# Performance work log

Hardware: AMD Instinct MI355X
Metric: run time of the kernel (lower is better)

## Reference

```python
import jax, jax.numpy as jnp
import numpy as np

B, N_OP, N_MA, F, H, O = 32, 512, 64, 8, 128, 8


def _lin(k, fan_in, fan_out):
    kw, kb = jax.random.split(k)
    bound = 1.0 / np.sqrt(fan_in)
    w = jax.random.uniform(kw, (fan_in, fan_out), jnp.float32, -bound, bound)
    b = jax.random.uniform(kb, (fan_out,), jnp.float32, -bound, bound)
    return w, b


def setup_inputs() -> dict:
    key = jax.random.key(0)
    ks = jax.random.split(key, 12)
    inp = {
        "ope_ma_adj_batch": jax.random.randint(ks[0], (B, N_OP, N_MA), 0, 2, dtype=jnp.int32),
        "feats_op": jax.random.normal(ks[1], (B, N_OP, F), jnp.float32),
        "feats_ma": jax.random.normal(ks[2], (B, N_MA, F), jnp.float32),
    }
    # MLPsim 0 (machine aggregation): Linear(F,H), Linear(H,H), Linear(H,O)
    inp["l0_w1"], inp["l0_b1"] = _lin(ks[3], F, H)
    inp["l0_w2"], inp["l0_b2"] = _lin(ks[4], H, H)
    inp["l0_w3"], inp["l0_b3"] = _lin(ks[5], H, O)
    # MLPsim 1 (self-loop aggregation)
    inp["l1_w1"], inp["l1_b1"] = _lin(ks[6], F, H)
    inp["l1_w2"], inp["l1_b2"] = _lin(ks[7], H, H)
    inp["l1_w3"], inp["l1_b3"] = _lin(ks[8], H, O)
    # Final project: Linear(2*O,H), Linear(H,H), Linear(H,O)
    inp["p_w1"], inp["p_b1"] = _lin(ks[9], 2 * O, H)
    inp["p_w2"], inp["p_b2"] = _lin(ks[10], H, H)
    inp["p_w3"], inp["p_b3"] = _lin(ks[11], H, O)
    return inp


def _mlp3(x, w1, b1, w2, b2, w3, b3):
    # Linear -> ELU -> Linear -> ELU -> Linear (matches nn.Sequential in MLPsim.project)
    x = jax.nn.elu(x @ w1 + b1)
    x = jax.nn.elu(x @ w2 + b2)
    return x @ w3 + b3


def reference(ope_ma_adj_batch, feats_op, feats_ma,
              l0_w1, l0_b1, l0_w2, l0_b2, l0_w3, l0_b3,
              l1_w1, l1_b1, l1_w2, l1_b2, l1_w3, l1_b3,
              p_w1, p_b1, p_w2, p_b2, p_w3, p_b3):
    # MLPsim: adj.unsqueeze(-1)*feat.unsqueeze(-3) then sum(-2) == adj @ feat
    adj = ope_ma_adj_batch.astype(feats_ma.dtype)
    agg_ma = jnp.einsum('bnm,bmf->bnf', adj, feats_ma)       # (B, N_op, F)
    emb0 = _mlp3(agg_ma, l0_w1, l0_b1, l0_w2, l0_b2, l0_w3, l0_b3)
    # Second adjacency is the identity self-loop: I @ feats_op == feats_op
    emb1 = _mlp3(feats_op, l1_w1, l1_b1, l1_w2, l1_b2, l1_w3, l1_b3)
    cat = jnp.concatenate([emb0, emb1], axis=-1)              # (B, N_op, 2*O)
    # Final project: ELU -> Linear -> ELU -> Linear -> ELU -> Linear
    mu = _mlp3(jax.nn.elu(cat), p_w1, p_b1, p_w2, p_b2, p_w3, p_b3)
    return mu
```

## Files before the change

kernel.cpp:

```cpp
#include <hip/hip_runtime.h>

#define BB    32
#define N_OPC 512
#define N_MAC 64
#define FF    8
#define HH    128
#define OO    8
#define TM    32
#define ASTRB 136

typedef _Float16 f16x8 __attribute__((ext_vector_type(8)));
typedef _Float16 f16x4 __attribute__((ext_vector_type(4)));
typedef float    f32x4 __attribute__((ext_vector_type(4)));

#define WS_W2 0
#define WS_W3 49152
#define WS_W1 55296

__device__ __forceinline__ float elu_f(float x) {
    return x > 0.0f ? x : (__expf(x) - 1.0f);
}
__device__ __forceinline__ void store_f16(float v, ushort* dst, int off) {
    const _Float16 h = (_Float16)v;
    dst[off] = __builtin_bit_cast(ushort, h);
}

__global__ void prep_kernel(const float* __restrict__ w20, const float* __restrict__ w21,
                            const float* __restrict__ w22,
                            const float* __restrict__ w30, const float* __restrict__ w31,
                            const float* __restrict__ w32,
                            const float* __restrict__ w10, const float* __restrict__ w11,
                            const float* __restrict__ w12,
                            ushort* __restrict__ ws)
{
    const int gid = blockIdx.x * 256 + threadIdx.x;
    if (gid < 3 * 16384) {
        const int layer = gid >> 14, idx = gid & 16383;
        const float* w = layer == 0 ? w20 : layer == 1 ? w21 : w22;
        const int k = idx >> 7, j = idx & 127;
        const float x = w[idx];
        const int ks = k >> 5, kk = k & 31, jt = j >> 4, jj = j & 15;
        const int lane = ((kk >> 3) << 4) | jj, i = kk & 7;
        const int off = (((jt * 4 + ks) * 64 + lane) << 3) + i;
        const _Float16 h = (_Float16)x;
        ws[WS_W2 + layer * 16384 + off] = __builtin_bit_cast(ushort, h);
    } else if (gid < 3 * 16384 + 3 * 2048) {
        const int g2 = gid - 3 * 16384;
        const int layer = g2 >> 11, idx = g2 & 2047;
        const float* w = layer == 0 ? w30 : layer == 1 ? w31 : w32;
        const int i = idx & 7, lane = (idx >> 3) & 63, ks = idx >> 9;
        const int k = ks * 32 + (lane >> 4) * 8 + i, j = lane & 15;
        const float x = (j < OO) ? w[k * OO + j] : 0.0f;
        const _Float16 h = (_Float16)x;
        ws[WS_W3 + layer * 2048 + idx] = __builtin_bit_cast(ushort, h);
    } else {
        const int g1 = gid - (3 * 16384 + 3 * 2048);
        const int layer = g1 >> 12, idx = g1 & 4095;
        const float* w = layer == 0 ? w10 : layer == 1 ? w11 : w12;
        const int i = idx & 7, lane = (idx >> 3) & 63, jt = idx >> 9;
        const int k = (lane >> 4) * 8 + i, j = jt * 16 + (lane & 15);
        const int Kr = (layer == 2) ? 16 : 8;
        const float x = (k < Kr) ? w[k * HH + j] : 0.0f;
        const _Float16 h = (_Float16)x;
        ws[WS_W1 + layer * 4096 + idx] = __builtin_bit_cast(ushort, h);
    }
}

__device__ __forceinline__ void epi_store(f32x4 a, const float* __restrict__ bias, int jb,
                                          ushort* __restrict__ dst, int off)
{
    const float4 bb = *(const float4*)(bias + jb);
    f16x4 v;
    v[0] = (_Float16)elu_f(a[0] + bb.x);
    v[1] = (_Float16)elu_f(a[1] + bb.y);
    v[2] = (_Float16)elu_f(a[2] + bb.z);
    v[3] = (_Float16)elu_f(a[3] + bb.w);
    *(f16x4*)(dst + off) = v;
}

__global__ __launch_bounds__(512, 4) void mlps_kernel(
    const int*   __restrict__ adj,
    const float* __restrict__ fop,
    const float* __restrict__ fmab,
    const float* __restrict__ l0b1, const float* __restrict__ l0b2, const float* __restrict__ l0b3,
    const float* __restrict__ l1b1, const float* __restrict__ l1b2, const float* __restrict__ l1b3,
    const float* __restrict__ pb1,  const float* __restrict__ pb2,  const float* __restrict__ pb3,
    const ushort* __restrict__ wsf,
    float* __restrict__ out)
{
    __shared__ __align__(16) ushort hbuf[2][TM * ASTRB];
    __shared__ __align__(16) ushort gbuf[2][TM * ASTRB];
    __shared__ float fmS[N_MAC * FF];
    __shared__ __align__(16) ushort xinF[TM * FF];
    __shared__ __align__(16) ushort xopF[TM * FF];
    __shared__ __align__(16) ushort catF[TM * 16];

    const int tid  = threadIdx.x;
    const int wv   = tid >> 6;
    const int lane = tid & 63;
    const int lrow = lane & 15;
    const int lk   = lane >> 4;
    const int row0 = blockIdx.x * TM;
    const int b    = row0 / N_OPC;

    fmS[tid] = fmab[b * N_MAC * FF + tid];
    if (tid < TM * FF)
        store_f16(fop[row0 * FF + tid], xopF, tid);
    __syncthreads();

    if (tid < TM * FF) {
        const int r = tid >> 3, f = tid & 7;
        const int* arow = adj + (row0 + r) * N_MAC;
        float a = 0.0f;
        #pragma unroll
        for (int m4 = 0; m4 < N_MAC; m4 += 4) {
            const int4 av = *(const int4*)(arow + m4);
            a = fmaf((float)av.x, fmS[(m4 + 0) * FF + f], a);
            a = fmaf((float)av.y, fmS[(m4 + 1) * FF + f], a);
            a = fmaf((float)av.z, fmS[(m4 + 2) * FF + f], a);
            a = fmaf((float)av.w, fmS[(m4 + 3) * FF + f], a);
        }
        store_f16(a, xinF, tid);
    }
    __syncthreads();

    {
        const int br = wv >> 2, jt0 = (wv & 3) * 2;
        const ushort* xF = br ? xopF : xinF;
        const f16x8* WF = (const f16x8*)(wsf + WS_W1 + br * 4096);
        const float* b1 = br ? l1b1 : l0b1;
        f16x8 X[2] = {};
        if (lk == 0) {
            #pragma unroll
            for (int rt = 0; rt < 2; ++rt)
                X[rt] = *(const f16x8*)(xF + (rt * 16 + lrow) * 8);
        }
        f32x4 acc[2][2] = {};
        #pragma unroll
        for (int jtl = 0; jtl < 2; ++jtl) {
            const f16x8 wh = WF[(jt0 + jtl) * 64 + lane];
            #pragma unroll
            for (int rt = 0; rt < 2; ++rt)
                acc[jtl][rt] = __builtin_amdgcn_mfma_f32_16x16x32_f16(wh, X[rt], acc[jtl][rt], 0, 0, 0);
        }
        ushort* dF = hbuf[br];
        #pragma unroll
        for (int jtl = 0; jtl < 2; ++jtl) {
            const int jb = (jt0 + jtl) * 16 + lk * 4;
            #pragma unroll
            for (int rt = 0; rt < 2; ++rt)
                epi_store(acc[jtl][rt], b1, jb, dF, (rt * 16 + lrow) * ASTRB + jb);
        }
    }
    __syncthreads();

    {
        const int br = wv >> 2, jt0 = (wv & 3) * 2;
        const ushort* aF = hbuf[br];
        const f16x8* WF = (const f16x8*)(wsf + WS_W2 + br * 16384);
        f32x4 acc[2][2] = {};
        #pragma unroll
        for (int ks = 0; ks < 4; ++ks) {
            f16x8 x[2];
            #pragma unroll
            for (int rt = 0; rt < 2; ++rt)
                x[rt] = *(const f16x8*)(aF + (rt * 16 + lrow) * ASTRB + ks * 32 + lk * 8);
            #pragma unroll
            for (int jtl = 0; jtl < 2; ++jtl) {
                const f16x8 wh = WF[((jt0 + jtl) * 4 + ks) * 64 + lane];
                #pragma unroll
                for (int rt = 0; rt < 2; ++rt)
                    acc[jtl][rt] = __builtin_amdgcn_mfma_f32_16x16x32_f16(wh, x[rt], acc[jtl][rt], 0, 0, 0);
            }
        }
        const float* b2 = br ? l1b2 : l0b2;
        ushort* dF = gbuf[br];
        #pragma unroll
        for (int jtl = 0; jtl < 2; ++jtl) {
            const int jb = (jt0 + jtl) * 16 + lk * 4;
            #pragma unroll
            for (int rt = 0; rt < 2; ++rt)
                epi_store(acc[jtl][rt], b2, jb, dF, (rt * 16 + lrow) * ASTRB + jb);
        }
    }
    __syncthreads();

    if (wv < 4) {
        const int br = wv >> 1, rt = wv & 1;
        const ushort* aF = gbuf[br];
        const f16x8* WF = (const f16x8*)(wsf + WS_W3 + br * 2048);
        f32x4 acc = {};
        #pragma unroll
        for (int ks = 0; ks < 4; ++ks) {
            const f16x8 x = *(const f16x8*)(aF + (rt * 16 + lrow) * ASTRB + ks * 32 + lk * 8);
            const f16x8 wh = WF[ks * 64 + lane];
            acc = __builtin_amdgcn_mfma_f32_16x16x32_f16(wh, x, acc, 0, 0, 0);
        }
        if (lk < 2) {
            const float* b3 = br ? l1b3 : l0b3;
            epi_store(acc, b3, lk * 4, catF, (rt * 16 + lrow) * 16 + br * OO + lk * 4);
        }
    }
    __syncthreads();

    {
        const f16x8* WF = (const f16x8*)(wsf + WS_W1 + 2 * 4096);
        f16x8 X[2] = {};
        if (lk < 2) {
            #pragma unroll
            for (int rt = 0; rt < 2; ++rt)
                X[rt] = *(const f16x8*)(catF + (rt * 16 + lrow) * 16 + lk * 8);
        }
        f32x4 acc[2] = {};
        const f16x8 wh = WF[wv * 64 + lane];
        #pragma unroll
        for (int rt = 0; rt < 2; ++rt)
            acc[rt] = __builtin_amdgcn_mfma_f32_16x16x32_f16(wh, X[rt], acc[rt], 0, 0, 0);
        const int jb = wv * 16 + lk * 4;
        #pragma unroll
        for (int rt = 0; rt < 2; ++rt)
            epi_store(acc[rt], pb1, jb, hbuf[0], (rt * 16 + lrow) * ASTRB + jb);
    }
    __syncthreads();

    {
        const ushort* aF = hbuf[0];
        const f16x8* WF = (const f16x8*)(wsf + WS_W2 + 2 * 16384);
        f32x4 acc[2] = {};
        #pragma unroll
        for (int ks = 0; ks < 4; ++ks) {
            const f16x8 wh = WF[(wv * 4 + ks) * 64 + lane];
            #pragma unroll
            for (int rt = 0; rt < 2; ++rt) {
                const f16x8 x = *(const f16x8*)(aF + (rt * 16 + lrow) * ASTRB + ks * 32 + lk * 8);
                acc[rt] = __builtin_amdgcn_mfma_f32_16x16x32_f16(wh, x, acc[rt], 0, 0, 0);
            }
        }
        const int jb = wv * 16 + lk * 4;
        #pragma unroll
        for (int rt = 0; rt < 2; ++rt)
            epi_store(acc[rt], pb2, jb, gbuf[0], (rt * 16 + lrow) * ASTRB + jb);
    }
    __syncthreads();

    if (wv < 2) {
        const int rt = wv;
        const ushort* aF = gbuf[0];
        const f16x8* WF = (const f16x8*)(wsf + WS_W3 + 2 * 2048);
        f32x4 acc = {};
        #pragma unroll
        for (int ks = 0; ks < 4; ++ks) {
            const f16x8 x = *(const f16x8*)(aF + (rt * 16 + lrow) * ASTRB + ks * 32 + lk * 8);
            const f16x8 wh = WF[ks * 64 + lane];
            acc = __builtin_amdgcn_mfma_f32_16x16x32_f16(wh, x, acc, 0, 0, 0);
        }
        if (lk < 2) {
            const float4 bb = *(const float4*)(pb3 + lk * 4);
            float4 o;
            o.x = acc[0] + bb.x; o.y = acc[1] + bb.y;
            o.z = acc[2] + bb.z; o.w = acc[3] + bb.w;
            *(float4*)(out + (row0 + rt * 16 + lrow) * OO + lk * 4) = o;
        }
    }
}

extern "C" void kernel_launch(void* const* d_in, const int* in_sizes, int n_in,
                              void* d_out, int out_size, void* d_ws, size_t ws_size,
                              hipStream_t stream) {
    (void)in_sizes; (void)n_in; (void)out_size; (void)ws_size;
    const int*   adj  = (const int*)  d_in[0];
    const float* fop  = (const float*)d_in[1];
    const float* fmab = (const float*)d_in[2];
    const float* l0w1 = (const float*)d_in[3];
    const float* l0b1 = (const float*)d_in[4];
    const float* l0w2 = (const float*)d_in[5];
    const float* l0b2 = (const float*)d_in[6];
    const float* l0w3 = (const float*)d_in[7];
    const float* l0b3 = (const float*)d_in[8];
    const float* l1w1 = (const float*)d_in[9];
    const float* l1b1 = (const float*)d_in[10];
    const float* l1w2 = (const float*)d_in[11];
    const float* l1b2 = (const float*)d_in[12];
    const float* l1w3 = (const float*)d_in[13];
    const float* l1b3 = (const float*)d_in[14];
    const float* pw1  = (const float*)d_in[15];
    const float* pb1  = (const float*)d_in[16];
    const float* pw2  = (const float*)d_in[17];
    const float* pb2  = (const float*)d_in[18];
    const float* pw3  = (const float*)d_in[19];
    const float* pb3  = (const float*)d_in[20];
    float* out = (float*)d_out;
    ushort* wsf = (ushort*)d_ws;

    prep_kernel<<<dim3(264), dim3(256), 0, stream>>>(
        l0w2, l1w2, pw2, l0w3, l1w3, pw3, l0w1, l1w1, pw1, wsf);

    const int grid = (BB * N_OPC) / TM;
    mlps_kernel<<<dim3(grid), dim3(512), 0, stream>>>(
        adj, fop, fmab,
        l0b1, l0b2, l0b3,
        l1b1, l1b2, l1b3,
        pb1, pb2, pb3,
        wsf, out);
}
```

Before: 18.47 us.

## Fold machine features into first layer weights and prefetch weights into registers

The prep kernel now precomputes feats_ma @ W1 for each batch as an f16 fragment, so branch 0's first layer becomes a direct MFMA of the adjacency (converted to f16) against that product. This removes the scalar aggregation loop, the shared-memory staging of feats and two barriers. Weight fragments for later layers are loaded into registers one stage early so the global loads overlap the previous stage. In exchange the prep kernel does more work (about 1000 blocks), register pressure rises, and the reassociated sum is rounded to f16 before use.

Result: no change. 18.78 us (+1.7%).

```diff
diff --git a/kernel.cpp b/kernel.cpp
--- a/kernel.cpp
+++ b/kernel.cpp
@@ -13,16 +13,14 @@
 typedef _Float16 f16x4 __attribute__((ext_vector_type(4)));
 typedef float    f32x4 __attribute__((ext_vector_type(4)));
 
-#define WS_W2 0
-#define WS_W3 49152
-#define WS_W1 55296
+#define WS_W2  0
+#define WS_W3  49152
+#define WS_W1  55296
+#define WS_FMW 67584
+#define PREP_ITEMS (67584 + BB * 8192)
 
 __device__ __forceinline__ float elu_f(float x) {
     return x > 0.0f ? x : (__expf(x) - 1.0f);
-}
-__device__ __forceinline__ void store_f16(float v, ushort* dst, int off) {
-    const _Float16 h = (_Float16)v;
-    dst[off] = __builtin_bit_cast(ushort, h);
 }
 
 __global__ void prep_kernel(const float* __restrict__ w20, const float* __restrict__ w21,
@@ -31,6 +29,7 @@
                             const float* __restrict__ w32,
                             const float* __restrict__ w10, const float* __restrict__ w11,
                             const float* __restrict__ w12,
+                            const float* __restrict__ fmab,
                             ushort* __restrict__ ws)
 {
     const int gid = blockIdx.x * 256 + threadIdx.x;
@@ -53,7 +52,7 @@
         const float x = (j < OO) ? w[k * OO + j] : 0.0f;
         const _Float16 h = (_Float16)x;
         ws[WS_W3 + layer * 2048 + idx] = __builtin_bit_cast(ushort, h);
-    } else {
+    } else if (gid < 67584) {
         const int g1 = gid - (3 * 16384 + 3 * 2048);
         const int layer = g1 >> 12, idx = g1 & 4095;
         const float* w = layer == 0 ? w10 : layer == 1 ? w11 : w12;
@@ -63,6 +62,19 @@
         const float x = (k < Kr) ? w[k * HH + j] : 0.0f;
         const _Float16 h = (_Float16)x;
         ws[WS_W1 + layer * 4096 + idx] = __builtin_bit_cast(ushort, h);
+    } else {
+        const int g = gid - WS_FMW;
+        const int bb = g >> 13, idx = g & 8191;
+        const int i = idx & 7, lane = (idx >> 3) & 63, fk = idx >> 9;
+        const int ks = fk & 1, jt = fk >> 1;
+        const int k = ks * 32 + (lane >> 4) * 8 + i;
+        const int j = jt * 16 + (lane & 15);
+        const float* fmr = fmab + bb * (N_MAC * FF) + k * FF;
+        float x = 0.0f;
+        #pragma unroll
+        for (int f = 0; f < FF; ++f) x = fmaf(fmr[f], w10[f * HH + j], x);
+        const _Float16 h = (_Float16)x;
+        ws[WS_FMW + g] = __builtin_bit_cast(ushort, h);
     }
 }
 
@@ -81,7 +93,6 @@
 __global__ __launch_bounds__(512, 4) void mlps_kernel(
     const int*   __restrict__ adj,
     const float* __restrict__ fop,
-    const float* __restrict__ fmab,
     const float* __restrict__ l0b1, const float* __restrict__ l0b2, const float* __restrict__ l0b3,
     const float* __restrict__ l1b1, const float* __restrict__ l1b2, const float* __restrict__ l1b3,
     const float* __restrict__ pb1,  const float* __restrict__ pb2,  const float* __restrict__ pb3,
@@ -90,9 +101,6 @@
 {
     __shared__ __align__(16) ushort hbuf[2][TM * ASTRB];
     __shared__ __align__(16) ushort gbuf[2][TM * ASTRB];
-    __shared__ float fmS[N_MAC * FF];
-    __shared__ __align__(16) ushort xinF[TM * FF];
-    __shared__ __align__(16) ushort xopF[TM * FF];
     __shared__ __align__(16) ushort catF[TM * 16];
 
     const int tid  = threadIdx.x;
@@ -102,62 +110,93 @@
     const int lk   = lane >> 4;
     const int row0 = blockIdx.x * TM;
     const int b    = row0 / N_OPC;
-
-    fmS[tid] = fmab[b * N_MAC * FF + tid];
-    if (tid < TM * FF)
-        store_f16(fop[row0 * FF + tid], xopF, tid);
-    __syncthreads();
-
-    if (tid < TM * FF) {
-        const int r = tid >> 3, f = tid & 7;
-        const int* arow = adj + (row0 + r) * N_MAC;
-        float a = 0.0f;
-        #pragma unroll
-        for (int m4 = 0; m4 < N_MAC; m4 += 4) {
-            const int4 av = *(const int4*)(arow + m4);
-            a = fmaf((float)av.x, fmS[(m4 + 0) * FF + f], a);
-            a = fmaf((float)av.y, fmS[(m4 + 1) * FF + f], a);
-            a = fmaf((float)av.z, fmS[(m4 + 2) * FF + f], a);
-            a = fmaf((float)av.w, fmS[(m4 + 3) * FF + f], a);
-        }
-        store_f16(a, xinF, tid);
-    }
-    __syncthreads();
-
-    {
-        const int br = wv >> 2, jt0 = (wv & 3) * 2;
-        const ushort* xF = br ? xopF : xinF;
-        const f16x8* WF = (const f16x8*)(wsf + WS_W1 + br * 4096);
-        const float* b1 = br ? l1b1 : l0b1;
+    const int br   = wv >> 2, jt0 = (wv & 3) * 2;
+
+    f32x4 acc1[2][2] = {};
+    if (br == 0) {
+        const f16x8* FMWF = (const f16x8*)(wsf + WS_FMW + b * 8192);
+        f16x8 wa[2][2];
+        #pragma unroll
+        for (int jtl = 0; jtl < 2; ++jtl)
+            #pragma unroll
+            for (int ks = 0; ks < 2; ++ks)
+                wa[jtl][ks] = FMWF[((jt0 + jtl) * 2 + ks) * 64 + lane];
+        f16x8 xb[2][2];
+        #pragma unroll
+        for (int rt = 0; rt < 2; ++rt)
+            #pragma unroll
+            for (int ks = 0; ks < 2; ++ks) {
+                const int* ap = adj + (row0 + rt * 16 + lrow) * N_MAC + ks * 32 + lk * 8;
+                const int4 a0 = *(const int4*)ap;
+                const int4 a1 = *(const int4*)(ap + 4);
+                f16x8 v;
+                v[0] = (_Float16)a0.x; v[1] = (_Float16)a0.y;
+                v[2] = (_Float16)a0.z; v[3] = (_Float16)a0.w;
+                v[4] = (_Float16)a1.x; v[5] = (_Float16)a1.y;
+                v[6] = (_Float16)a1.z; v[7] = (_Float16)a1.w;
+                xb[rt][ks] = v;
+            }
+        #pragma unroll
+        for (int jtl = 0; jtl < 2; ++jtl)
+            #pragma unroll
+            for (int rt = 0; rt < 2; ++rt)
+                #pragma unroll
+                for (int ks = 0; ks < 2; ++ks)
+                    acc1[jtl][rt] = __builtin_amdgcn_mfma_f32_16x16x32_f16(wa[jtl][ks], xb[rt][ks], acc1[jtl][rt], 0, 0, 0);
+    } else {
+        const f16x8* WF = (const f16x8*)(wsf + WS_W1 + 4096);
+        const f16x8 w1a = WF[jt0 * 64 + lane];
+        const f16x8 w1b = WF[(jt0 + 1) * 64 + lane];
         f16x8 X[2] = {};
         if (lk == 0) {
             #pragma unroll
-            for (int rt = 0; rt < 2; ++rt)
-                X[rt] = *(const f16x8*)(xF + (rt * 16 + lrow) * 8);
-        }
-        f32x4 acc[2][2] = {};
-        #pragma unroll
-        for (int jtl = 0; jtl < 2; ++jtl) {
-            const f16x8 wh = WF[(jt0 + jtl) * 64 + lane];
-            #pragma unroll
-            for (int rt = 0; rt < 2; ++rt)
-                acc[jtl][rt] = __builtin_amdgcn_mfma_f32_16x16x32_f16(wh, X[rt], acc[jtl][rt], 0, 0, 0);
-        }
-        ushort* dF = hbuf[br];
+            for (int rt = 0; rt < 2; ++rt) {
+                const float* src = fop + (row0 + rt * 16 + lrow) * FF;
+                const float4 f0 = *(const float4*)src;
+                const float4 f1 = *(const float4*)(src + 4);
+                f16x8 v;
+                v[0] = (_Float16)f0.x; v[1] = (_Float16)f0.y;
+                v[2] = (_Float16)f0.z; v[3] = (_Float16)f0.w;
+                v[4] = (_Float16)f1.x; v[5] = (_Float16)f1.y;
+                v[6] = (_Float16)f1.z; v[7] = (_Float16)f1.w;
+                X[rt] = v;
+            }
+        }
+        #pragma unroll
+        for (int rt = 0; rt < 2; ++rt) {
+            acc1[0][rt] = __builtin_amdgcn_mfma_f32_16x16x32_f16(w1a, X[rt], acc1[0][rt], 0, 0, 0);
+            acc1[1][rt] = __builtin_amdgcn_mfma_f32_16x16x32_f16(w1b, X[rt], acc1[1][rt], 0, 0, 0);
+        }
+    }
+    f16x8 wf2[2][4];
+    {
+        const f16x8* W2F = (const f16x8*)(wsf + WS_W2 + br * 16384);
+        #pragma unroll
+        for (int jtl = 0; jtl < 2; ++jtl)
+            #pragma unroll
+            for (int ks = 0; ks < 4; ++ks)
+                wf2[jtl][ks] = W2F[((jt0 + jtl) * 4 + ks) * 64 + lane];
+    }
+    {
+        const float* b1 = br ? l1b1 : l0b1;
         #pragma unroll
         for (int jtl = 0; jtl < 2; ++jtl) {
             const int jb = (jt0 + jtl) * 16 + lk * 4;
             #pragma unroll
             for (int rt = 0; rt < 2; ++rt)
-                epi_store(acc[jtl][rt], b1, jb, dF, (rt * 16 + lrow) * ASTRB + jb);
-        }
-    }
-    __syncthreads();
-
-    {
-        const int br = wv >> 2, jt0 = (wv & 3) * 2;
+                epi_store(acc1[jtl][rt], b1, jb, hbuf[br], (rt * 16 + lrow) * ASTRB + jb);
+        }
+    }
+    __syncthreads();
+
+    f16x8 wf3[4];
+    if (wv < 4) {
+        const f16x8* WF3 = (const f16x8*)(wsf + WS_W3 + (wv >> 1) * 2048);
+        #pragma unroll
+        for (int ks = 0; ks < 4; ++ks) wf3[ks] = WF3[ks * 64 + lane];
+    }
+    {
         const ushort* aF = hbuf[br];
-        const f16x8* WF = (const f16x8*)(wsf + WS_W2 + br * 16384);
         f32x4 acc[2][2] = {};
         #pragma unroll
         for (int ks = 0; ks < 4; ++ks) {
@@ -166,45 +205,50 @@
             for (int rt = 0; rt < 2; ++rt)
                 x[rt] = *(const f16x8*)(aF + (rt * 16 + lrow) * ASTRB + ks * 32 + lk * 8);
             #pragma unroll
-            for (int jtl = 0; jtl < 2; ++jtl) {
-                const f16x8 wh = WF[((jt0 + jtl) * 4 + ks) * 64 + lane];
+            for (int jtl = 0; jtl < 2; ++jtl)
                 #pragma unroll
                 for (int rt = 0; rt < 2; ++rt)
-                    acc[jtl][rt] = __builtin_amdgcn_mfma_f32_16x16x32_f16(wh, x[rt], acc[jtl][rt], 0, 0, 0);
-            }
+                    acc[jtl][rt] = __builtin_amdgcn_mfma_f32_16x16x32_f16(wf2[jtl][ks], x[rt], acc[jtl][rt], 0, 0, 0);
         }
         const float* b2 = br ? l1b2 : l0b2;
-        ushort* dF = gbuf[br];
         #pragma unroll
         for (int jtl = 0; jtl < 2; ++jtl) {
             const int jb = (jt0 + jtl) * 16 + lk * 4;
             #pragma unroll
             for (int rt = 0; rt < 2; ++rt)
-                epi_store(acc[jtl][rt], b2, jb, dF, (rt * 16 + lrow) * ASTRB + jb);
-        }
-    }
-    __syncthreads();
-
+                epi_store(acc[jtl][rt], b2, jb, gbuf[br], (rt * 16 + lrow) * ASTRB + jb);
+        }
+    }
+    __syncthreads();
+
+    f16x8 wf4;
+    {
+        const f16x8* WF = (const f16x8*)(wsf + WS_W1 + 2 * 4096);
+        wf4 = WF[wv * 64 + lane];
+    }
     if (wv < 4) {
-        const int br = wv >> 1, rt = wv & 1;
-        const ushort* aF = gbuf[br];
-        const f16x8* WF = (const f16x8*)(wsf + WS_W3 + br * 2048);
+        const int br3 = wv >> 1, rt = wv & 1;
+        const ushort* aF = gbuf[br3];
         f32x4 acc = {};
         #pragma unroll
         for (int ks = 0; ks < 4; ++ks) {
             const f16x8 x = *(const f16x8*)(aF + (rt * 16 + lrow) * ASTRB + ks * 32 + lk * 8);
-            const f16x8 wh = WF[ks * 64 + lane];
-            acc = __builtin_amdgcn_mfma_f32_16x16x32_f16(wh, x, acc, 0, 0, 0);
+            acc = __builtin_amdgcn_mfma_f32_16x16x32_f16(wf3[ks], x, acc, 0, 0, 0);
         }
         if (lk < 2) {
-            const float* b3 = br ? l1b3 : l0b3;
-            epi_store(acc, b3, lk * 4, catF, (rt * 16 + lrow) * 16 + br * OO + lk * 4);
-        }
-    }
-    __syncthreads();
-
-    {
-        const f16x8* WF = (const f16x8*)(wsf + WS_W1 + 2 * 4096);
+            const float* b3 = br3 ? l1b3 : l0b3;
+            epi_store(acc, b3, lk * 4, catF, (rt * 16 + lrow) * 16 + br3 * OO + lk * 4);
+        }
+    }
+    __syncthreads();
+
+    f16x8 wf5[4];
+    {
+        const f16x8* WF = (const f16x8*)(wsf + WS_W2 + 2 * 16384);
+        #pragma unroll
+        for (int ks = 0; ks < 4; ++ks) wf5[ks] = WF[(wv * 4 + ks) * 64 + lane];
+    }
+    {
         f16x8 X[2] = {};
         if (lk < 2) {
             #pragma unroll
@@ -212,10 +256,9 @@
                 X[rt] = *(const f16x8*)(catF + (rt * 16 + lrow) * 16 + lk * 8);
         }
         f32x4 acc[2] = {};
-        const f16x8 wh = WF[wv * 64 + lane];
         #pragma unroll
         for (int rt = 0; rt < 2; ++rt)
-            acc[rt] = __builtin_amdgcn_mfma_f32_16x16x32_f16(wh, X[rt], acc[rt], 0, 0, 0);
+            acc[rt] = __builtin_amdgcn_mfma_f32_16x16x32_f16(wf4, X[rt], acc[rt], 0, 0, 0);
         const int jb = wv * 16 + lk * 4;
         #pragma unroll
         for (int rt = 0; rt < 2; ++rt)
@@ -223,17 +266,21 @@
     }
     __syncthreads();
 
+    f16x8 wf6[4];
+    if (wv < 2) {
+        const f16x8* WF = (const f16x8*)(wsf + WS_W3 + 2 * 2048);
+        #pragma unroll
+        for (int ks = 0; ks < 4; ++ks) wf6[ks] = WF[ks * 64 + lane];
+    }
     {
         const ushort* aF = hbuf[0];
-        const f16x8* WF = (const f16x8*)(wsf + WS_W2 + 2 * 16384);
         f32x4 acc[2] = {};
         #pragma unroll
         for (int ks = 0; ks < 4; ++ks) {
-            const f16x8 wh = WF[(wv * 4 + ks) * 64 + lane];
             #pragma unroll
             for (int rt = 0; rt < 2; ++rt) {
                 const f16x8 x = *(const f16x8*)(aF + (rt * 16 + lrow) * ASTRB + ks * 32 + lk * 8);
-                acc[rt] = __builtin_amdgcn_mfma_f32_16x16x32_f16(wh, x, acc[rt], 0, 0, 0);
+                acc[rt] = __builtin_amdgcn_mfma_f32_16x16x32_f16(wf5[ks], x, acc[rt], 0, 0, 0);
             }
         }
         const int jb = wv * 16 + lk * 4;
@@ -246,13 +293,11 @@
     if (wv < 2) {
         const int rt = wv;
         const ushort* aF = gbuf[0];
-        const f16x8* WF = (const f16x8*)(wsf + WS_W3 + 2 * 2048);
         f32x4 acc = {};
         #pragma unroll
         for (int ks = 0; ks < 4; ++ks) {
             const f16x8 x = *(const f16x8*)(aF + (rt * 16 + lrow) * ASTRB + ks * 32 + lk * 8);
-            const f16x8 wh = WF[ks * 64 + lane];
-            acc = __builtin_amdgcn_mfma_f32_16x16x32_f16(wh, x, acc, 0, 0, 0);
+            acc = __builtin_amdgcn_mfma_f32_16x16x32_f16(wf6[ks], x, acc, 0, 0, 0);
         }
         if (lk < 2) {
             const float4 bb = *(const float4*)(pb3 + lk * 4);
@@ -292,12 +337,13 @@
     float* out = (float*)d_out;
     ushort* wsf = (ushort*)d_ws;
 
-    prep_kernel<<<dim3(264), dim3(256), 0, stream>>>(
-        l0w2, l1w2, pw2, l0w3, l1w3, pw3, l0w1, l1w1, pw1, wsf);
+    const int prep_blocks = PREP_ITEMS / 256;
+    prep_kernel<<<dim3(prep_blocks), dim3(256), 0, stream>>>(
+        l0w2, l1w2, pw2, l0w3, l1w3, pw3, l0w1, l1w1, pw1, fmab, wsf);
 
     const int grid = (BB * N_OPC) / TM;
     mlps_kernel<<<dim3(grid), dim3(512), 0, stream>>>(
-        adj, fop, fmab,
+        adj, fop,
         l0b1, l0b2, l0b3,
         l1b1, l1b2, l1b3,
         pb1, pb2, pb3,
```

## Drop weight-prep kernel; gather fp32 weights into fp16 MFMA fragments in-kernel

Applied to the files above, without the earlier changes.

Removes the separate prep kernel that repacked weights into fp16 MFMA-fragment layout in the workspace. Each wave now gathers its weight fragments directly from the fp32 weight tensors with strided scalar loads and converts them to fp16. Most fragments are prefetched before the layer that uses them, and the layer-2 fragments are loaded before the adjacency aggregation. This saves one kernel launch and its serialization, but adds many uncoalesced strided global loads per block (512 blocks each re-gathering weights), plus more register pressure from holding the fragments.

New measurement: 17.77 us (median of 2 runs). 1.04x faster.

```diff
diff --git a/kernel.cpp b/kernel.cpp
--- a/kernel.cpp
+++ b/kernel.cpp
@@ -13,10 +13,6 @@
 typedef _Float16 f16x4 __attribute__((ext_vector_type(4)));
 typedef float    f32x4 __attribute__((ext_vector_type(4)));
 
-#define WS_W2 0
-#define WS_W3 49152
-#define WS_W1 55296
-
 __device__ __forceinline__ float elu_f(float x) {
     return x > 0.0f ? x : (__expf(x) - 1.0f);
 }
@@ -24,46 +20,12 @@
     const _Float16 h = (_Float16)v;
     dst[off] = __builtin_bit_cast(ushort, h);
 }
-
-__global__ void prep_kernel(const float* __restrict__ w20, const float* __restrict__ w21,
-                            const float* __restrict__ w22,
-                            const float* __restrict__ w30, const float* __restrict__ w31,
-                            const float* __restrict__ w32,
-                            const float* __restrict__ w10, const float* __restrict__ w11,
-                            const float* __restrict__ w12,
-                            ushort* __restrict__ ws)
-{
-    const int gid = blockIdx.x * 256 + threadIdx.x;
-    if (gid < 3 * 16384) {
-        const int layer = gid >> 14, idx = gid & 16383;
-        const float* w = layer == 0 ? w20 : layer == 1 ? w21 : w22;
-        const int k = idx >> 7, j = idx & 127;
-        const float x = w[idx];
-        const int ks = k >> 5, kk = k & 31, jt = j >> 4, jj = j & 15;
-        const int lane = ((kk >> 3) << 4) | jj, i = kk & 7;
-        const int off = (((jt * 4 + ks) * 64 + lane) << 3) + i;
-        const _Float16 h = (_Float16)x;
-        ws[WS_W2 + layer * 16384 + off] = __builtin_bit_cast(ushort, h);
-    } else if (gid < 3 * 16384 + 3 * 2048) {
-        const int g2 = gid - 3 * 16384;
-        const int layer = g2 >> 11, idx = g2 & 2047;
-        const float* w = layer == 0 ? w30 : layer == 1 ? w31 : w32;
-        const int i = idx & 7, lane = (idx >> 3) & 63, ks = idx >> 9;
-        const int k = ks * 32 + (lane >> 4) * 8 + i, j = lane & 15;
-        const float x = (j < OO) ? w[k * OO + j] : 0.0f;
-        const _Float16 h = (_Float16)x;
-        ws[WS_W3 + layer * 2048 + idx] = __builtin_bit_cast(ushort, h);
-    } else {
-        const int g1 = gid - (3 * 16384 + 3 * 2048);
-        const int layer = g1 >> 12, idx = g1 & 4095;
-        const float* w = layer == 0 ? w10 : layer == 1 ? w11 : w12;
-        const int i = idx & 7, lane = (idx >> 3) & 63, jt = idx >> 9;
-        const int k = (lane >> 4) * 8 + i, j = jt * 16 + (lane & 15);
-        const int Kr = (layer == 2) ? 16 : 8;
-        const float x = (k < Kr) ? w[k * HH + j] : 0.0f;
-        const _Float16 h = (_Float16)x;
-        ws[WS_W1 + layer * 4096 + idx] = __builtin_bit_cast(ushort, h);
-    }
+__device__ __forceinline__ f16x8 gather8(const float* __restrict__ w, int kbase, int j, int ld) {
+    f16x8 v;
+    #pragma unroll
+    for (int i = 0; i < 8; ++i)
+        v[i] = (_Float16)w[(kbase + i) * ld + j];
+    return v;
 }
 
 __device__ __forceinline__ void epi_store(f32x4 a, const float* __restrict__ bias, int jb,
@@ -82,10 +44,15 @@
     const int*   __restrict__ adj,
     const float* __restrict__ fop,
     const float* __restrict__ fmab,
-    const float* __restrict__ l0b1, const float* __restrict__ l0b2, const float* __restrict__ l0b3,
-    const float* __restrict__ l1b1, const float* __restrict__ l1b2, const float* __restrict__ l1b3,
-    const float* __restrict__ pb1,  const float* __restrict__ pb2,  const float* __restrict__ pb3,
-    const ushort* __restrict__ wsf,
+    const float* __restrict__ l0w1, const float* __restrict__ l0b1,
+    const float* __restrict__ l0w2, const float* __restrict__ l0b2,
+    const float* __restrict__ l0w3, const float* __restrict__ l0b3,
+    const float* __restrict__ l1w1, const float* __restrict__ l1b1,
+    const float* __restrict__ l1w2, const float* __restrict__ l1b2,
+    const float* __restrict__ l1w3, const float* __restrict__ l1b3,
+    const float* __restrict__ pw1,  const float* __restrict__ pb1,
+    const float* __restrict__ pw2,  const float* __restrict__ pb2,
+    const float* __restrict__ pw3,  const float* __restrict__ pb3,
     float* __restrict__ out)
 {
     __shared__ __align__(16) ushort hbuf[2][TM * ASTRB];
@@ -102,6 +69,21 @@
     const int lk   = lane >> 4;
     const int row0 = blockIdx.x * TM;
     const int b    = row0 / N_OPC;
+    const int br   = wv >> 2, jt0 = (wv & 3) * 2;
+
+    const float* w1p = br ? l1w1 : l0w1;
+    f16x8 w1f[2] = {};
+    if (lk == 0) {
+        w1f[0] = gather8(w1p, 0, jt0 * 16 + lrow, HH);
+        w1f[1] = gather8(w1p, 0, (jt0 + 1) * 16 + lrow, HH);
+    }
+    const float* w2p = br ? l1w2 : l0w2;
+    f16x8 wf2[2][4];
+    #pragma unroll
+    for (int jtl = 0; jtl < 2; ++jtl)
+        #pragma unroll
+        for (int ks = 0; ks < 4; ++ks)
+            wf2[jtl][ks] = gather8(w2p, ks * 32 + lk * 8, (jt0 + jtl) * 16 + lrow, HH);
 
     fmS[tid] = fmab[b * N_MAC * FF + tid];
     if (tid < TM * FF)
@@ -125,9 +107,7 @@
     __syncthreads();
 
     {
-        const int br = wv >> 2, jt0 = (wv & 3) * 2;
         const ushort* xF = br ? xopF : xinF;
-        const f16x8* WF = (const f16x8*)(wsf + WS_W1 + br * 4096);
         const float* b1 = br ? l1b1 : l0b1;
         f16x8 X[2] = {};
         if (lk == 0) {
@@ -137,27 +117,29 @@
         }
         f32x4 acc[2][2] = {};
         #pragma unroll
-        for (int jtl = 0; jtl < 2; ++jtl) {
-            const f16x8 wh = WF[(jt0 + jtl) * 64 + lane];
-            #pragma unroll
-            for (int rt = 0; rt < 2; ++rt)
-                acc[jtl][rt] = __builtin_amdgcn_mfma_f32_16x16x32_f16(wh, X[rt], acc[jtl][rt], 0, 0, 0);
-        }
-        ushort* dF = hbuf[br];
+        for (int jtl = 0; jtl < 2; ++jtl)
+            #pragma unroll
+            for (int rt = 0; rt < 2; ++rt)
+                acc[jtl][rt] = __builtin_amdgcn_mfma_f32_16x16x32_f16(w1f[jtl], X[rt], acc[jtl][rt], 0, 0, 0);
         #pragma unroll
         for (int jtl = 0; jtl < 2; ++jtl) {
             const int jb = (jt0 + jtl) * 16 + lk * 4;
             #pragma unroll
             for (int rt = 0; rt < 2; ++rt)
-                epi_store(acc[jtl][rt], b1, jb, dF, (rt * 16 + lrow) * ASTRB + jb);
-        }
-    }
-    __syncthreads();
-
-    {
-        const int br = wv >> 2, jt0 = (wv & 3) * 2;
+                epi_store(acc[jtl][rt], b1, jb, hbuf[br], (rt * 16 + lrow) * ASTRB + jb);
+        }
+    }
+    __syncthreads();
+
+    f16x8 wf3[4] = {};
+    if (wv < 4 && lrow < OO) {
+        const float* w3p = (wv >> 1) ? l1w3 : l0w3;
+        #pragma unroll
+        for (int ks = 0; ks < 4; ++ks)
+            wf3[ks] = gather8(w3p, ks * 32 + lk * 8, lrow, OO);
+    }
+    {
         const ushort* aF = hbuf[br];
-        const f16x8* WF = (const f16x8*)(wsf + WS_W2 + br * 16384);
         f32x4 acc[2][2] = {};
         #pragma unroll
         for (int ks = 0; ks < 4; ++ks) {
@@ -166,45 +148,46 @@
             for (int rt = 0; rt < 2; ++rt)
                 x[rt] = *(const f16x8*)(aF + (rt * 16 + lrow) * ASTRB + ks * 32 + lk * 8);
             #pragma unroll
-            for (int jtl = 0; jtl < 2; ++jtl) {
-                const f16x8 wh = WF[((jt0 + jtl) * 4 + ks) * 64 + lane];
+            for (int jtl = 0; jtl < 2; ++jtl)
                 #pragma unroll
                 for (int rt = 0; rt < 2; ++rt)
-                    acc[jtl][rt] = __builtin_amdgcn_mfma_f32_16x16x32_f16(wh, x[rt], acc[jtl][rt], 0, 0, 0);
-            }
+                    acc[jtl][rt] = __builtin_amdgcn_mfma_f32_16x16x32_f16(wf2[jtl][ks], x[rt], acc[jtl][rt], 0, 0, 0);
         }
         const float* b2 = br ? l1b2 : l0b2;
-        ushort* dF = gbuf[br];
         #pragma unroll
         for (int jtl = 0; jtl < 2; ++jtl) {
             const int jb = (jt0 + jtl) * 16 + lk * 4;
             #pragma unroll
             for (int rt = 0; rt < 2; ++rt)
-                epi_store(acc[jtl][rt], b2, jb, dF, (rt * 16 + lrow) * ASTRB + jb);
-        }
-    }
-    __syncthreads();
-
+                epi_store(acc[jtl][rt], b2, jb, gbuf[br], (rt * 16 + lrow) * ASTRB + jb);
+        }
+    }
+    __syncthreads();
+
+    f16x8 wf4 = {};
+    if (lk < 2)
+        wf4 = gather8(pw1, lk * 8, wv * 16 + lrow, HH);
     if (wv < 4) {
-        const int br = wv >> 1, rt = wv & 1;
-        const ushort* aF = gbuf[br];
-        const f16x8* WF = (const f16x8*)(wsf + WS_W3 + br * 2048);
+        const int br3 = wv >> 1, rt = wv & 1;
+        const ushort* aF = gbuf[br3];
         f32x4 acc = {};
         #pragma unroll
         for (int ks = 0; ks < 4; ++ks) {
             const f16x8 x = *(const f16x8*)(aF + (rt * 16 + lrow) * ASTRB + ks * 32 + lk * 8);
-            const f16x8 wh = WF[ks * 64 + lane];
-            acc = __builtin_amdgcn_mfma_f32_16x16x32_f16(wh, x, acc, 0, 0, 0);
+            acc = __builtin_amdgcn_mfma_f32_16x16x32_f16(wf3[ks], x, acc, 0, 0, 0);
         }
         if (lk < 2) {
-            const float* b3 = br ? l1b3 : l0b3;
-            epi_store(acc, b3, lk * 4, catF, (rt * 16 + lrow) * 16 + br * OO + lk * 4);
-        }
-    }
-    __syncthreads();
-
-    {
-        const f16x8* WF = (const f16x8*)(wsf + WS_W1 + 2 * 4096);
+            const float* b3 = br3 ? l1b3 : l0b3;
+            epi_store(acc, b3, lk * 4, catF, (rt * 16 + lrow) * 16 + br3 * OO + lk * 4);
+        }
+    }
+    __syncthreads();
+
+    f16x8 wf5[4];
+    #pragma unroll
+    for (int ks = 0; ks < 4; ++ks)
+        wf5[ks] = gather8(pw2, ks * 32 + lk * 8, wv * 16 + lrow, HH);
+    {
         f16x8 X[2] = {};
         if (lk < 2) {
             #pragma unroll
@@ -212,10 +195,9 @@
                 X[rt] = *(const f16x8*)(catF + (rt * 16 + lrow) * 16 + lk * 8);
         }
         f32x4 acc[2] = {};
-        const f16x8 wh = WF[wv * 64 + lane];
         #pragma unroll
         for (int rt = 0; rt < 2; ++rt)
-            acc[rt] = __builtin_amdgcn_mfma_f32_16x16x32_f16(wh, X[rt], acc[rt], 0, 0, 0);
+            acc[rt] = __builtin_amdgcn_mfma_f32_16x16x32_f16(wf4, X[rt], acc[rt], 0, 0, 0);
         const int jb = wv * 16 + lk * 4;
         #pragma unroll
         for (int rt = 0; rt < 2; ++rt)
@@ -223,17 +205,21 @@
     }
     __syncthreads();
 
+    f16x8 wf6[4] = {};
+    if (wv < 2 && lrow < OO) {
+        #pragma unroll
+        for (int ks = 0; ks < 4; ++ks)
+            wf6[ks] = gather8(pw3, ks * 32 + lk * 8, lrow, OO);
+    }
     {
         const ushort* aF = hbuf[0];
-        const f16x8* WF = (const f16x8*)(wsf + WS_W2 + 2 * 16384);
         f32x4 acc[2] = {};
         #pragma unroll
         for (int ks = 0; ks < 4; ++ks) {
-            const f16x8 wh = WF[(wv * 4 + ks) * 64 + lane];
             #pragma unroll
             for (int rt = 0; rt < 2; ++rt) {
                 const f16x8 x = *(const f16x8*)(aF + (rt * 16 + lrow) * ASTRB + ks * 32 + lk * 8);
-                acc[rt] = __builtin_amdgcn_mfma_f32_16x16x32_f16(wh, x, acc[rt], 0, 0, 0);
+                acc[rt] = __builtin_amdgcn_mfma_f32_16x16x32_f16(wf5[ks], x, acc[rt], 0, 0, 0);
             }
         }
         const int jb = wv * 16 + lk * 4;
@@ -246,13 +232,11 @@
     if (wv < 2) {
         const int rt = wv;
         const ushort* aF = gbuf[0];
-        const f16x8* WF = (const f16x8*)(wsf + WS_W3 + 2 * 2048);
         f32x4 acc = {};
         #pragma unroll
         for (int ks = 0; ks < 4; ++ks) {
             const f16x8 x = *(const f16x8*)(aF + (rt * 16 + lrow) * ASTRB + ks * 32 + lk * 8);
-            const f16x8 wh = WF[ks * 64 + lane];
-            acc = __builtin_amdgcn_mfma_f32_16x16x32_f16(wh, x, acc, 0, 0, 0);
+            acc = __builtin_amdgcn_mfma_f32_16x16x32_f16(wf6[ks], x, acc, 0, 0, 0);
         }
         if (lk < 2) {
             const float4 bb = *(const float4*)(pb3 + lk * 4);
@@ -267,7 +251,7 @@
 extern "C" void kernel_launch(void* const* d_in, const int* in_sizes, int n_in,
                               void* d_out, int out_size, void* d_ws, size_t ws_size,
                               hipStream_t stream) {
-    (void)in_sizes; (void)n_in; (void)out_size; (void)ws_size;
+    (void)in_sizes; (void)n_in; (void)out_size; (void)d_ws; (void)ws_size;
     const int*   adj  = (const int*)  d_in[0];
     const float* fop  = (const float*)d_in[1];
     const float* fmab = (const float*)d_in[2];
@@ -290,16 +274,12 @@
     const float* pw3  = (const float*)d_in[19];
     const float* pb3  = (const float*)d_in[20];
     float* out = (float*)d_out;
-    ushort* wsf = (ushort*)d_ws;
-
-    prep_kernel<<<dim3(264), dim3(256), 0, stream>>>(
-        l0w2, l1w2, pw2, l0w3, l1w3, pw3, l0w1, l1w1, pw1, wsf);
 
     const int grid = (BB * N_OPC) / TM;
     mlps_kernel<<<dim3(grid), dim3(512), 0, stream>>>(
         adj, fop, fmab,
-        l0b1, l0b2, l0b3,
-        l1b1, l1b2, l1b3,
-        pb1, pb2, pb3,
-        wsf, out);
-}
+        l0w1, l0b1, l0w2, l0b2, l0w3, l0b3,
+        l1w1, l1b1, l1w2, l1b2, l1w3, l1b3,
+        pw1, pb1, pw2, pb2, pw3, pb3,
+        out);
+}
```
